# Kernel optimization log

Measured on AMD Instinct MI355X. Metric: run time of the kernel, lower is better.

Reference implementation:

```python
import jax, jax.numpy as jnp
import numpy as np
from functools import partial

K_NEIGHBORS = 9
GRID = 28            # hard-coded in AnomalyMapGenerator
OUT_HW = (224, 224)  # input_size
SIGMA = 4
RADIUS = int(4.0 * SIGMA + 0.5)  # scipy gaussian_filter truncate=4 -> 16


def avg_pool3(x):
    # torch.nn.AvgPool2d(3, 1, 1), count_include_pad=True -> window sum / 9
    s = jax.lax.reduce_window(x, 0.0, jax.lax.add, (1, 1, 3, 3), (1, 1, 1, 1),
                              [(0, 0), (0, 0), (1, 1), (1, 1)])
    return s / 9.0


def gaussian_filter2d(img):
    # scipy.ndimage.gaussian_filter, sigma=4, mode='reflect' (== numpy 'symmetric')
    xs = jnp.arange(-RADIUS, RADIUS + 1, dtype=img.dtype)
    k = jnp.exp(-(xs ** 2) / (2.0 * SIGMA * SIGMA))
    k = k / k.sum()
    conv = lambda v: jnp.convolve(v, k, mode='valid')
    p = jnp.pad(img, ((RADIUS, RADIUS), (0, 0)), mode='symmetric')
    img = jax.vmap(conv, in_axes=1, out_axes=1)(p)
    p = jnp.pad(img, ((0, 0), (RADIUS, RADIUS)), mode='symmetric')
    img = jax.vmap(conv, in_axes=0, out_axes=0)(p)
    return img


def setup_inputs() -> dict:
    key = jax.random.key(0)
    k1, k2, k3 = jax.random.split(key, 3)
    return {
        'features_layer2': jax.random.normal(k1, (1, 512, 28, 28), jnp.float32),
        'features_layer3': jax.random.normal(k2, (1, 1024, 14, 14), jnp.float32),
        'memory_bank': jax.random.normal(k3, (100000, 1536), jnp.float32),
    }


def reference(features_layer2, features_layer3, memory_bank):
    # 1) feature pooling (AvgPool2d(3,1,1)) per layer
    f2 = avg_pool3(features_layer2)   # [1, 512, 28, 28]
    f3 = avg_pool3(features_layer3)   # [1, 1024, 14, 14]

    # 2) concat_layer_embedding: unfold/fold == nearest-neighbor upsample + channel concat
    s = f2.shape[2] // f3.shape[2]    # stride = 2
    f3_up = jnp.repeat(jnp.repeat(f3, s, axis=2), s, axis=3)   # [1,1024,28,28]
    embedding = jnp.concatenate([f2, f3_up], axis=1)           # [1,1536,28,28]

    # 3) reshape_embedding: [B,E,H,W] -> [B*H*W, E]
    E = embedding.shape[1]
    emb = embedding.transpose(0, 2, 3, 1).reshape(-1, E)       # [784, 1536]

    # 4) brute-force kNN (euclidean) against memory bank, k=9
    d2 = (jnp.sum(emb * emb, axis=1, keepdims=True)
          + jnp.sum(memory_bank * memory_bank, axis=1)[None, :]
          - 2.0 * emb @ memory_bank.T)                         # [784, N]
    neg_top, _ = jax.lax.top_k(-d2, K_NEIGHBORS)               # smallest distances
    patch_scores = jnp.sqrt(jnp.clip(-neg_top, 1e-12))         # [784, 9]

    # 5) anomaly map: reshape 28x28 -> bilinear resize -> gaussian blur
    amap = patch_scores[:, 0].reshape(GRID, GRID)
    amap = jax.image.resize(amap, OUT_HW, method='bilinear')
    anomaly_map = gaussian_filter2d(amap)

    # 6) image-level anomaly score
    col0 = patch_scores[:, 0]
    conf = patch_scores[jnp.argmax(col0)]                      # [9]
    e = jnp.exp(conf)
    weight = 1.0 - jnp.max(e) / jnp.sum(e)
    anomaly_score = weight * jnp.max(col0)

    return anomaly_map, anomaly_score
```

## Files before the change

kernel.cpp:

```cpp
#include <hip/hip_runtime.h>

#define INFV 1e30f

typedef __attribute__((ext_vector_type(8))) short bf16x8;
typedef __attribute__((ext_vector_type(16))) float f32x16;

__device__ __forceinline__ unsigned short f2bf(float f){
  union { float f; unsigned u; } v; v.f = f;
  unsigned r = v.u + 0x7FFFu + ((v.u >> 16) & 1u);
  return (unsigned short)(r >> 16);
}
__device__ __forceinline__ float bf2f(unsigned short b){
  union { unsigned u; float f; } v; v.u = ((unsigned)b) << 16;
  return v.f;
}
__device__ __forceinline__ void async_cp16(void* lds, const void* g){
  __builtin_amdgcn_global_load_lds((const __attribute__((address_space(1))) unsigned int*)g,
                                   (__attribute__((address_space(3))) unsigned int*)lds,
                                   16, 0, 0);
}

__global__ void k_pool(const float* __restrict__ f2, const float* __restrict__ f3,
                       float* __restrict__ pf2, float* __restrict__ pf3){
  const int idx = blockIdx.x*256 + threadIdx.x;
  if (idx < 512*784){
    const int c = idx / 784, rem = idx % 784, y = rem / 28, x = rem % 28;
    const float* base = f2 + c*784;
    float s = 0.f;
    for (int dy = -1; dy <= 1; ++dy){
      int yy = y + dy; if (yy < 0 || yy > 27) continue;
      for (int dx = -1; dx <= 1; ++dx){
        int xx = x + dx; if (xx < 0 || xx > 27) continue;
        s += base[yy*28 + xx];
      }
    }
    pf2[idx] = s * (1.0f/9.0f);
  } else {
    const int j = idx - 512*784;
    if (j < 1024*196){
      const int c = j / 196, rem = j % 196, y = rem / 14, x = rem % 14;
      const float* base = f3 + c*196;
      float s = 0.f;
      for (int dy = -1; dy <= 1; ++dy){
        int yy = y + dy; if (yy < 0 || yy > 13) continue;
        for (int dx = -1; dx <= 1; ++dx){
          int xx = x + dx; if (xx < 0 || xx > 13) continue;
          s += base[yy*14 + xx];
        }
      }
      pf3[j] = s * (1.0f/9.0f);
    }
  }
}

__global__ void k_emb(const float* __restrict__ pf2, const float* __restrict__ pf3,
                      unsigned short* __restrict__ Aw, float* __restrict__ en2){
  __shared__ float red[256];
  const int p = blockIdx.x;
  const int t = threadIdx.x;
  const int y = p / 28, x = p % 28;
  float a2 = 0.f;
  for (int it = 0; it < 6; ++it){
    const int k = it*256 + t;
    float v = 0.f;
    if (p < 784){
      if (k < 512) v = pf2[k*784 + y*28 + x];
      else         v = pf3[(k - 512)*196 + (y >> 1)*14 + (x >> 1)];
    }
    a2 += v*v;
    const int chunk = k >> 5, kq = (k >> 3) & 3, j = k & 7;
    Aw[(size_t)chunk*26624 + (size_t)(kq*832 + p)*8 + j] = f2bf(v);
  }
  red[t] = a2;
  __syncthreads();
  for (int s = 128; s > 0; s >>= 1){
    if (t < s) red[t] += red[t + s];
    __syncthreads();
  }
  if (t == 0) en2[p] = red[0];
}

__global__ __launch_bounds__(768, 3) void k_gemm(const float* __restrict__ bank,
                                                 const unsigned short* __restrict__ Aw,
                                                 const float* __restrict__ en2,
                                                 float* __restrict__ pmin){
  __shared__ short As[2][26624];
  __shared__ short Bs[2][2048];
  __shared__ float Bf[2][2048];
  __shared__ float en2s[832];
  __shared__ float bn2p[512];
  __shared__ float bn2v[64];

  const int tid = threadIdx.x;
  const int w = tid >> 6;
  const int lane = tid & 63;
  const int hi = lane >> 5;
  const int ln = lane & 31;
  const int n0 = blockIdx.x * 64;
  const int rm = (w < 2) ? 3 : 2;

  for (int i = tid; i < 832; i += 768) en2s[i] = en2[i];

  f32x16 acc[3][2];
  #pragma unroll
  for (int i = 0; i < 3; ++i)
    #pragma unroll
    for (int j = 0; j < 2; ++j)
      #pragma unroll
      for (int g = 0; g < 16; ++g) acc[i][j][g] = 0.0f;

  const int brow = tid >> 3;
  const int bpart = tid & 7;
  const bool bth = (tid < 512);
  const bool bvalid = bth && (n0 + brow < 100000);
  const float* bp = bank + (size_t)(n0 + brow) * 1536 + bpart * 4;
  const int bslot = ((bpart >> 1) * 64 + brow) * 8 + (bpart & 1) * 4;
  float s2 = 0.0f;

  const int row0 = w*64 + ln;
  const int row2 = 768 + w*32 + ln;

  if (bvalid) async_cp16(&Bf[0][tid*4], bp);
  {
    const unsigned short* Ag = Aw;
    #pragma unroll
    for (int it = 0; it < 5; ++it){
      int u = it*768 + tid;
      if (u < 3328) async_cp16(&As[0][u*8], Ag + (size_t)u*8);
    }
  }
  __syncthreads();
  if (bth){
    float4 bv = make_float4(0.f, 0.f, 0.f, 0.f);
    if (bvalid) bv = *(const float4*)&Bf[0][tid*4];
    s2 += bv.x*bv.x + bv.y*bv.y + bv.z*bv.z + bv.w*bv.w;
    short4 sv;
    sv.x = (short)f2bf(bv.x); sv.y = (short)f2bf(bv.y);
    sv.z = (short)f2bf(bv.z); sv.w = (short)f2bf(bv.w);
    *(short4*)&Bs[0][bslot] = sv;
  }
  __syncthreads();

  int cur = 0;
  for (int r = 0; r < 48; ++r){
    const int nxt = cur ^ 1;
    if (r < 47){
      if (bvalid) async_cp16(&Bf[nxt][tid*4], bp + (r+1)*32);
      const unsigned short* Ag = Aw + (size_t)(r+1) * 26624;
      #pragma unroll
      for (int it = 0; it < 5; ++it){
        int u = it*768 + tid;
        if (u < 3328) async_cp16(&As[nxt][u*8], Ag + (size_t)u*8);
      }
    }
    const short* Ac = As[cur];
    const short* Bc = Bs[cur];
    #pragma unroll
    for (int s = 0; s < 2; ++s){
      const int kq = s*2 + hi;
      bf16x8 b0 = *(const bf16x8*)&Bc[(kq*64 + ln)*8];
      bf16x8 b1 = *(const bf16x8*)&Bc[(kq*64 + 32 + ln)*8];
      #pragma unroll
      for (int i = 0; i < 3; ++i){
        if (i < rm){
          const int rr = (i < 2) ? (row0 + i*32) : row2;
          bf16x8 a = *(const bf16x8*)&Ac[(kq*832 + rr)*8];
          acc[i][0] = __builtin_amdgcn_mfma_f32_32x32x16_bf16(a, b0, acc[i][0], 0, 0, 0);
          acc[i][1] = __builtin_amdgcn_mfma_f32_32x32x16_bf16(a, b1, acc[i][1], 0, 0, 0);
        }
      }
    }
    __syncthreads();
    if (r < 47 && bth){
      float4 bv = make_float4(0.f, 0.f, 0.f, 0.f);
      if (bvalid) bv = *(const float4*)&Bf[nxt][tid*4];
      s2 += bv.x*bv.x + bv.y*bv.y + bv.z*bv.z + bv.w*bv.w;
      short4 sv;
      sv.x = (short)f2bf(bv.x); sv.y = (short)f2bf(bv.y);
      sv.z = (short)f2bf(bv.z); sv.w = (short)f2bf(bv.w);
      *(short4*)&Bs[nxt][bslot] = sv;
    }
    __syncthreads();
    cur = nxt;
  }

  if (bth) bn2p[tid] = s2;
  __syncthreads();
  if (tid < 64){
    float t0 = 0.f;
    #pragma unroll
    for (int j = 0; j < 8; ++j) t0 += bn2p[tid*8 + j];
    bn2v[tid] = (n0 + tid < 100000) ? t0 : INFV;
  }
  __syncthreads();

  #pragma unroll
  for (int i = 0; i < 3; ++i){
    if (i < rm){
      const int mb = (i < 2) ? (w*64 + i*32) : (768 + w*32);
      float vv[16];
      #pragma unroll
      for (int g = 0; g < 16; ++g){
        const int m = mb + (g & 3) + 8*(g >> 2) + 4*hi;
        const float e2 = en2s[m];
        float d0 = e2 + bn2v[ln]      - 2.0f*acc[i][0][g];
        float d1 = e2 + bn2v[32 + ln] - 2.0f*acc[i][1][g];
        float v = fminf(d0, d1);
        #pragma unroll
        for (int off = 1; off < 32; off <<= 1)
          v = fminf(v, __shfl_xor(v, off, 64));
        vv[g] = v;
      }
      if (ln == 0){
        #pragma unroll
        for (int g = 0; g < 16; ++g){
          const int m = mb + (g & 3) + 8*(g >> 2) + 4*hi;
          pmin[(size_t)blockIdx.x * 832 + m] = vv[g];
        }
      }
    }
  }
}

__global__ void k_colmin(const float* __restrict__ pmin, float* __restrict__ col0){
  __shared__ float red[256];
  const int t = threadIdx.x;
  const int m0 = blockIdx.x * 64;
  const int m = m0 + (t & 63);
  const int g = t >> 6;
  float v = INFV;
  for (int b = g; b < 1563; b += 4) v = fminf(v, pmin[(size_t)b*832 + m]);
  red[t] = v;
  __syncthreads();
  if (t < 64){
    float vv = fminf(fminf(red[t], red[64+t]), fminf(red[128+t], red[192+t]));
    col0[m0 + t] = sqrtf(fmaxf(vv, 1e-12f));
  }
}

__global__ void k_argmax(const float* __restrict__ col0,
                         const float* __restrict__ pmin,
                         float* __restrict__ scal){
  __shared__ float red[256];
  __shared__ int redi[256];
  __shared__ float cand[1563];
  const int t = threadIdx.x;

  float best = -INFV; int bi = 0x7FFFFFFF;
  for (int m = t; m < 784; m += 256){
    float v = col0[m];
    if (v > best){ best = v; bi = m; }
  }
  red[t] = best; redi[t] = bi;
  __syncthreads();
  for (int s = 128; s > 0; s >>= 1){
    if (t < s){
      if (red[t+s] > red[t] || (red[t+s] == red[t] && redi[t+s] < redi[t])){
        red[t] = red[t+s]; redi[t] = redi[t+s];
      }
    }
    __syncthreads();
  }
  const int r = redi[0];
  const float maxv = red[0];
  __syncthreads();

  for (int b = t; b < 1563; b += 256) cand[b] = pmin[(size_t)b*832 + r];
  __syncthreads();

  float b9 = 0.f;
  for (int it = 0; it < 9; ++it){
    float lb = INFV; int li = -1;
    for (int b = t; b < 1563; b += 256){
      float v = cand[b];
      if (v < lb){ lb = v; li = b; }
    }
    red[t] = lb; redi[t] = li;
    __syncthreads();
    for (int s = 128; s > 0; s >>= 1){
      if (t < s && red[t+s] < red[t]){ red[t] = red[t+s]; redi[t] = redi[t+s]; }
      __syncthreads();
    }
    b9 = red[0];
    if (t == 0 && redi[0] >= 0) cand[redi[0]] = INFV;
    __syncthreads();
  }
  if (t == 0){
    ((int*)scal)[0] = r;
    scal[1] = maxv;
    scal[2] = b9 + 1.0f;
  }
}

__global__ void k_cand(const float* __restrict__ bank,
                       const unsigned short* __restrict__ Aw,
                       const float* __restrict__ en2,
                       const float* __restrict__ pmin,
                       const float* __restrict__ scal,
                       float* __restrict__ d2row){
  const int bid = blockIdx.x;
  const int t = threadIdx.x;
  const int r = ((const int*)scal)[0];
  const float thr = scal[2];
  const int n0 = bid * 64;

  if (pmin[(size_t)bid*832 + r] > thr){
    if (t < 64) d2row[n0 + t] = INFV;
    return;
  }
  __shared__ short er[1536];
  for (int k = t; k < 1536; k += 256){
    const int chunk = k >> 5, kq = (k >> 3) & 3, j = k & 7;
    er[k] = Aw[(size_t)chunk*26624 + (size_t)(kq*832 + r)*8 + j];
  }
  __syncthreads();
  const float e2r = en2[r];
  const int wv = t >> 6, ln = t & 63;
  for (int i = 0; i < 16; ++i){
    const int nl = wv*16 + i;
    const int n = n0 + nl;
    float dot = 0.f, b2 = 0.f;
    if (n < 100000){
      const float* bp2 = bank + (size_t)n * 1536;
      for (int k = ln; k < 1536; k += 64){
        float b = bp2[k];
        b2 += b*b;
        dot += bf2f(er[k]) * bf2f(f2bf(b));
      }
    }
    #pragma unroll
    for (int off = 1; off < 64; off <<= 1){
      dot += __shfl_xor(dot, off, 64);
      b2  += __shfl_xor(b2,  off, 64);
    }
    if (ln == 0) d2row[n] = (n < 100000) ? (e2r + b2 - 2.0f*dot) : INFV;
  }
}

__global__ void k_score(const float* __restrict__ d2row,
                        const float* __restrict__ scal,
                        float* __restrict__ outs){
  __shared__ float cs[2304];
  __shared__ float red[256];
  __shared__ int redi[256];
  __shared__ float nine[9];
  const int t = threadIdx.x;
  float loc[9];
  #pragma unroll
  for (int q = 0; q < 9; ++q) loc[q] = INFV;
  for (int n = t; n < 100000; n += 256){
    float v = d2row[n];
    if (v < loc[8]){
      loc[8] = v;
      #pragma unroll
      for (int q = 8; q > 0; --q){
        float a = fminf(loc[q-1], loc[q]);
        float b = fmaxf(loc[q-1], loc[q]);
        loc[q-1] = a; loc[q] = b;
      }
    }
  }
  #pragma unroll
  for (int q = 0; q < 9; ++q) cs[t*9 + q] = loc[q];
  __syncthreads();
  for (int it = 0; it < 9; ++it){
    float lb = INFV; int li = -1;
    for (int jx = t; jx < 2304; jx += 256){
      float v = cs[jx];
      if (v < lb){ lb = v; li = jx; }
    }
    red[t] = lb; redi[t] = li;
    __syncthreads();
    for (int s = 128; s > 0; s >>= 1){
      if (t < s && red[t+s] < red[t]){ red[t] = red[t+s]; redi[t] = redi[t+s]; }
      __syncthreads();
    }
    if (t == 0){ nine[it] = red[0]; if (redi[0] >= 0) cs[redi[0]] = INFV; }
    __syncthreads();
  }
  if (t == 0){
    float s[9];
    #pragma unroll
    for (int q = 0; q < 9; ++q) s[q] = sqrtf(fmaxf(nine[q], 1e-12f));
    const float mx = s[8];
    float sum = 0.f;
    #pragma unroll
    for (int q = 0; q < 9; ++q) sum += expf(s[q] - mx);
    const float weight = 1.0f - 1.0f/sum;
    outs[0] = weight * scal[1];
  }
}

__global__ void k_vblur(const float* __restrict__ col0, float* __restrict__ vmap){
  __shared__ float am[784];
  __shared__ float kw[33];
  const int t = threadIdx.x;
  for (int q = t; q < 784; q += 256) am[q] = col0[q];
  if (t < 33){ float d = (float)t - 16.0f; kw[t] = expf(-d*d*(1.0f/32.0f)); }
  __syncthreads();
  if (t == 0){
    float ss = 0.f;
    for (int q = 0; q < 33; ++q) ss += kw[q];
    const float inv = 1.0f/ss;
    for (int q = 0; q < 33; ++q) kw[q] *= inv;
  }
  __syncthreads();
  const int id = blockIdx.x*256 + t;
  const int i = id / 224, j = id % 224;
  const float ux = (j + 0.5f)*0.125f - 0.5f;
  const float fx0 = floorf(ux);
  const float fx = ux - fx0;
  int x0 = (int)fx0; int x1 = x0 + 1;
  x0 = max(0, min(27, x0)); x1 = max(0, min(27, x1));
  float a = 0.f;
  for (int d = 0; d < 33; ++d){
    int ii = i + d - 16;
    ii = (ii < 0) ? (-1 - ii) : ((ii > 223) ? (447 - ii) : ii);
    const float uy = (ii + 0.5f)*0.125f - 0.5f;
    const float fy0 = floorf(uy);
    const float fy = uy - fy0;
    int y0 = (int)fy0; int y1 = y0 + 1;
    y0 = max(0, min(27, y0)); y1 = max(0, min(27, y1));
    const float top = (1.0f - fx)*am[y0*28 + x0] + fx*am[y0*28 + x1];
    const float bot = (1.0f - fx)*am[y1*28 + x0] + fx*am[y1*28 + x1];
    a += kw[d]*((1.0f - fy)*top + fy*bot);
  }
  vmap[id] = a;
}

__global__ void k_hblur(const float* __restrict__ vmap, float* __restrict__ outm){
  __shared__ float rowb[256];
  __shared__ float kw[33];
  const int i = blockIdx.x;
  const int t = threadIdx.x;
  if (t < 33){ float d = (float)t - 16.0f; kw[t] = expf(-d*d*(1.0f/32.0f)); }
  __syncthreads();
  if (t == 0){
    float ss = 0.f;
    for (int q = 0; q < 33; ++q) ss += kw[q];
    const float inv = 1.0f/ss;
    for (int q = 0; q < 33; ++q) kw[q] *= inv;
  }
  int c = t - 16;
  c = (c < 0) ? (-1 - c) : ((c > 223) ? (447 - c) : c);
  rowb[t] = vmap[i*224 + c];
  __syncthreads();
  if (t < 224){
    float a = 0.f;
    #pragma unroll
    for (int d = 0; d < 33; ++d) a += kw[d]*rowb[t + d];
    outm[i*224 + t] = a;
  }
}

extern "C" void kernel_launch(void* const* d_in, const int* in_sizes, int n_in,
                              void* d_out, int out_size, void* d_ws, size_t ws_size,
                              hipStream_t stream) {
  const float* f2   = (const float*)d_in[0];
  const float* f3   = (const float*)d_in[1];
  const float* bank = (const float*)d_in[2];
  float* out = (float*)d_out;

  char* ws = (char*)d_ws;
  size_t off = 0;
  auto alloc = [&](size_t bytes) -> void* {
    void* p = ws + off;
    off += (bytes + 255) & ~(size_t)255;
    return p;
  };
  float* pf2           = (float*)alloc((size_t)512*784*4);
  float* pf3           = (float*)alloc((size_t)1024*196*4);
  unsigned short* A_ws = (unsigned short*)alloc((size_t)48*26624*2);
  float* en2           = (float*)alloc(832*4);
  float* pmin          = (float*)alloc((size_t)1563*832*4);
  float* col0          = (float*)alloc(832*4);
  float* scal          = (float*)alloc(64);
  float* d2row         = (float*)alloc(100032*4);
  float* vmap          = (float*)alloc((size_t)50176*4);

  k_pool  <<<2352, 256, 0, stream>>>(f2, f3, pf2, pf3);
  k_emb   <<<832,  256, 0, stream>>>(pf2, pf3, A_ws, en2);
  k_gemm  <<<1563, 768, 0, stream>>>(bank, A_ws, en2, pmin);
  k_colmin<<<13,   256, 0, stream>>>(pmin, col0);
  k_argmax<<<1,    256, 0, stream>>>(col0, pmin, scal);
  k_cand  <<<1563, 256, 0, stream>>>(bank, A_ws, en2, pmin, scal, d2row);
  k_score <<<1,    256, 0, stream>>>(d2row, scal, out + 50176);
  k_vblur <<<196,  256, 0, stream>>>(col0, vmap);
  k_hblur <<<224,  256, 0, stream>>>(vmap, out);
}
```

Before: 1.598 ms.

## Load A fragments directly from global into registers, dropping LDS staging

The query-embedding (A) tile is no longer staged through shared memory with async copies. Each wave now loads its own bf16 A fragments from global/L2 straight into registers, software-pipelined one half-chunk ahead. This frees about 104KB of LDS per block, which could allow more resident blocks, and removes the A copy traffic. The cost is that every block re-reads A from L2 with no reuse across waves, and global-load latency now sits in front of the MFMAs.

```diff
diff --git a/kernel.cpp b/kernel.cpp
--- a/kernel.cpp
+++ b/kernel.cpp
@@ -84,7 +84,6 @@
                                                  const unsigned short* __restrict__ Aw,
                                                  const float* __restrict__ en2,
                                                  float* __restrict__ pmin){
-  __shared__ short As[2][26624];
   __shared__ short Bs[2][2048];
   __shared__ float Bf[2][2048];
   __shared__ float en2s[832];
@@ -119,16 +118,15 @@
 
   const int row0 = w*64 + ln;
   const int row2 = 768 + w*32 + ln;
+  const unsigned short* pA0 = Aw + (size_t)(hi*832 + row0)*8;
+  const unsigned short* pA2 = Aw + (size_t)(hi*832 + row2)*8;
+
+  bf16x8 a0[3], a1[3];
 
   if (bvalid) async_cp16(&Bf[0][tid*4], bp);
-  {
-    const unsigned short* Ag = Aw;
-    #pragma unroll
-    for (int it = 0; it < 5; ++it){
-      int u = it*768 + tid;
-      if (u < 3328) async_cp16(&As[0][u*8], Ag + (size_t)u*8);
-    }
-  }
+  a0[0] = *(const bf16x8*)(pA0);
+  a0[1] = *(const bf16x8*)(pA0 + 256);
+  if (rm == 3) a0[2] = *(const bf16x8*)(pA2);
   __syncthreads();
   if (bth){
     float4 bv = make_float4(0.f, 0.f, 0.f, 0.f);
@@ -142,32 +140,42 @@
   __syncthreads();
 
   int cur = 0;
+  size_t coff = 0;
   for (int r = 0; r < 48; ++r){
     const int nxt = cur ^ 1;
     if (r < 47){
       if (bvalid) async_cp16(&Bf[nxt][tid*4], bp + (r+1)*32);
-      const unsigned short* Ag = Aw + (size_t)(r+1) * 26624;
-      #pragma unroll
-      for (int it = 0; it < 5; ++it){
-        int u = it*768 + tid;
-        if (u < 3328) async_cp16(&As[nxt][u*8], Ag + (size_t)u*8);
-      }
-    }
-    const short* Ac = As[cur];
-    const short* Bc = Bs[cur];
-    #pragma unroll
-    for (int s = 0; s < 2; ++s){
-      const int kq = s*2 + hi;
-      bf16x8 b0 = *(const bf16x8*)&Bc[(kq*64 + ln)*8];
-      bf16x8 b1 = *(const bf16x8*)&Bc[(kq*64 + 32 + ln)*8];
-      #pragma unroll
-      for (int i = 0; i < 3; ++i){
-        if (i < rm){
-          const int rr = (i < 2) ? (row0 + i*32) : row2;
-          bf16x8 a = *(const bf16x8*)&Ac[(kq*832 + rr)*8];
-          acc[i][0] = __builtin_amdgcn_mfma_f32_32x32x16_bf16(a, b0, acc[i][0], 0, 0, 0);
-          acc[i][1] = __builtin_amdgcn_mfma_f32_32x32x16_bf16(a, b1, acc[i][1], 0, 0, 0);
-        }
+    }
+    a1[0] = *(const bf16x8*)(pA0 + coff + 13312);
+    a1[1] = *(const bf16x8*)(pA0 + coff + 13312 + 256);
+    if (rm == 3) a1[2] = *(const bf16x8*)(pA2 + coff + 13312);
+    {
+      bf16x8 b0 = *(const bf16x8*)&Bs[cur][(hi*64 + ln)*8];
+      bf16x8 b1 = *(const bf16x8*)&Bs[cur][(hi*64 + 32 + ln)*8];
+      acc[0][0] = __builtin_amdgcn_mfma_f32_32x32x16_bf16(a0[0], b0, acc[0][0], 0, 0, 0);
+      acc[0][1] = __builtin_amdgcn_mfma_f32_32x32x16_bf16(a0[0], b1, acc[0][1], 0, 0, 0);
+      acc[1][0] = __builtin_amdgcn_mfma_f32_32x32x16_bf16(a0[1], b0, acc[1][0], 0, 0, 0);
+      acc[1][1] = __builtin_amdgcn_mfma_f32_32x32x16_bf16(a0[1], b1, acc[1][1], 0, 0, 0);
+      if (rm == 3){
+        acc[2][0] = __builtin_amdgcn_mfma_f32_32x32x16_bf16(a0[2], b0, acc[2][0], 0, 0, 0);
+        acc[2][1] = __builtin_amdgcn_mfma_f32_32x32x16_bf16(a0[2], b1, acc[2][1], 0, 0, 0);
+      }
+    }
+    if (r < 47){
+      a0[0] = *(const bf16x8*)(pA0 + coff + 26624);
+      a0[1] = *(const bf16x8*)(pA0 + coff + 26624 + 256);
+      if (rm == 3) a0[2] = *(const bf16x8*)(pA2 + coff + 26624);
+    }
+    {
+      bf16x8 b0 = *(const bf16x8*)&Bs[cur][((2 + hi)*64 + ln)*8];
+      bf16x8 b1 = *(const bf16x8*)&Bs[cur][((2 + hi)*64 + 32 + ln)*8];
+      acc[0][0] = __builtin_amdgcn_mfma_f32_32x32x16_bf16(a1[0], b0, acc[0][0], 0, 0, 0);
+      acc[0][1] = __builtin_amdgcn_mfma_f32_32x32x16_bf16(a1[0], b1, acc[0][1], 0, 0, 0);
+      acc[1][0] = __builtin_amdgcn_mfma_f32_32x32x16_bf16(a1[1], b0, acc[1][0], 0, 0, 0);
+      acc[1][1] = __builtin_amdgcn_mfma_f32_32x32x16_bf16(a1[1], b1, acc[1][1], 0, 0, 0);
+      if (rm == 3){
+        acc[2][0] = __builtin_amdgcn_mfma_f32_32x32x16_bf16(a1[2], b0, acc[2][0], 0, 0, 0);
+        acc[2][1] = __builtin_amdgcn_mfma_f32_32x32x16_bf16(a1[2], b1, acc[2][1], 0, 0, 0);
       }
     }
     __syncthreads();
@@ -182,6 +190,7 @@
     }
     __syncthreads();
     cur = nxt;
+    coff += 26624;
   }
 
   if (bth) bn2p[tid] = s2;
```

New measurement: 1.536 ms. 3.9% less time.
